# Optimization experiments

Measured on AMD Instinct MI355X. Metric: run time of the kernel, lower is better.

The kernel has to match this reference:

```python
import jax, jax.numpy as jnp
import numpy as np

N_NODES = 50000
N_EDGES = 800000
F_IN = 32      # node_features
F_OUT = 64     # out_channels
K = 3          # filter_size (diffusion steps)
PERIODS = 12


def dconv(X, edge_index, edge_weight, weight, bias):
    """torch_geometric_temporal DConv: dual-direction K-step diffusion conv.
    weight: (2, K, C_in, C_out); direction 0 = out-degree walk, 1 = in-degree walk.
    """
    N = X.shape[0]
    row, col = edge_index[0], edge_index[1]
    # Weighted degrees (edge_weight only enters via degree normalization,
    # matching the original implementation's message = norm * x_j).
    deg_out = jax.ops.segment_sum(edge_weight, row, num_segments=N)
    deg_in = jax.ops.segment_sum(edge_weight, col, num_segments=N)
    norm_out = (1.0 / deg_out)[row]  # [E], rows always have an out-edge here
    norm_in = (1.0 / deg_in)[col]    # [E]

    def prop_fwd(h):  # aggregate along edges src->dst
        return jax.ops.segment_sum(norm_out[:, None] * h[row], col, num_segments=N)

    def prop_rev(h):  # aggregate along reversed edges dst->src
        return jax.ops.segment_sum(norm_in[:, None] * h[col], row, num_segments=N)

    nK = weight.shape[1]
    Tx_0 = X
    H = X @ weight[0, 0] + X @ weight[1, 0]
    if nK > 1:
        Tx_1_o = prop_fwd(X)
        Tx_1_i = prop_rev(X)
        H = H + Tx_1_o @ weight[0, 1] + Tx_1_i @ weight[1, 1]
    for k in range(2, nK):
        Tx_2_o = 2.0 * prop_fwd(Tx_1_o) - Tx_0
        Tx_2_i = 2.0 * prop_rev(Tx_1_i) - Tx_0
        H = H + Tx_2_o @ weight[0, k] + Tx_2_i @ weight[1, k]
        Tx_0, Tx_1_o, Tx_1_i = Tx_1_o, Tx_2_o, Tx_2_i
    return H + bias


def setup_inputs() -> dict:
    key = jax.random.key(0)
    ks = jax.random.split(key, 12)
    C = F_IN + F_OUT  # DConv input channels = cat([X, H])
    s_conv = 1.0 / np.sqrt(C)
    s_lin = 1.0 / np.sqrt(F_OUT)
    return {
        "x": jax.random.normal(ks[0], (N_NODES, F_IN), dtype=jnp.float32),
        "edge_index": jax.random.randint(ks[1], (2, N_EDGES), 0, N_NODES, dtype=jnp.int64) if jax.config.jax_enable_x64 else jax.random.randint(ks[1], (2, N_EDGES), 0, N_NODES, dtype=jnp.int32),
        "edge_weight": jax.random.uniform(ks[2], (N_EDGES,), dtype=jnp.float32, minval=0.05, maxval=1.0),
        "w_z": jax.random.normal(ks[3], (2, K, C, F_OUT), dtype=jnp.float32) * s_conv,
        "b_z": jax.random.normal(ks[4], (F_OUT,), dtype=jnp.float32) * 0.01,
        "w_r": jax.random.normal(ks[5], (2, K, C, F_OUT), dtype=jnp.float32) * s_conv,
        "b_r": jax.random.normal(ks[6], (F_OUT,), dtype=jnp.float32) * 0.01,
        "w_h": jax.random.normal(ks[7], (2, K, C, F_OUT), dtype=jnp.float32) * s_conv,
        "b_h": jax.random.normal(ks[8], (F_OUT,), dtype=jnp.float32) * 0.01,
        "w_lin": jax.random.normal(ks[9], (F_OUT, PERIODS), dtype=jnp.float32) * s_lin,
        "b_lin": jax.random.normal(ks[10], (PERIODS,), dtype=jnp.float32) * s_lin,
    }


def reference(x, edge_index, edge_weight, w_z, b_z, w_r, b_r, w_h, b_h, w_lin, b_lin):
    # DCRNN cell with H0 = zeros (single call, no prior hidden state)
    H0 = jnp.zeros((x.shape[0], F_OUT), dtype=x.dtype)
    xh = jnp.concatenate([x, H0], axis=1)
    Z = jax.nn.sigmoid(dconv(xh, edge_index, edge_weight, w_z, b_z))
    R = jax.nn.sigmoid(dconv(xh, edge_index, edge_weight, w_r, b_r))
    xhr = jnp.concatenate([x, H0 * R], axis=1)
    H_tilde = jnp.tanh(dconv(xhr, edge_index, edge_weight, w_h, b_h))
    H = Z * H0 + (1.0 - Z) * H_tilde
    # ReLU + Linear head
    return jax.nn.relu(H) @ w_lin + b_lin
```

## Files before the change

### kernel.cpp

```cpp
#include <hip/hip_runtime.h>

#define N_NODES 50000
#define N_EDGES 800000
#define F_IN    32
#define F_OUT   64
#define PERIODS 12
#define C_FEAT  160

#define NKEY    (2 * N_NODES)
#define NBIN    782
#define NBLK_A  128
#define EPB     (N_EDGES / NBLK_A)
#define TOT     (2 * N_EDGES)
#define SCANA_N (NBIN * NBLK_A)
#define SCANA_NB 391
#define KPB     16
#define NBLK_DIR (N_NODES / KPB)
#define NF      ((size_t)N_NODES * F_IN)

typedef __attribute__((ext_vector_type(8))) short s16x8;
typedef __attribute__((ext_vector_type(4))) float f32x4;

static __device__ __forceinline__ ushort f2bf(float f) {
    unsigned u = __float_as_uint(f);
    unsigned r = (u + 0x7FFFu + ((u >> 16) & 1u)) >> 16;
    return (ushort)r;
}
static __device__ __forceinline__ float bfLO(unsigned h) {
    return __uint_as_float(h << 16);
}
static __device__ __forceinline__ float bfHI(unsigned h) {
    return __uint_as_float(h & 0xffff0000u);
}

static __device__ __forceinline__ s16x8 pack8(float4 lo, float4 hi) {
    s16x8 r;
    r[0] = (short)f2bf(lo.x); r[1] = (short)f2bf(lo.y);
    r[2] = (short)f2bf(lo.z); r[3] = (short)f2bf(lo.w);
    r[4] = (short)f2bf(hi.x); r[5] = (short)f2bf(hi.y);
    r[6] = (short)f2bf(hi.z); r[7] = (short)f2bf(hi.w);
    return r;
}

__global__ __launch_bounds__(256) void k_histA(const int* __restrict__ ei,
                                               int* __restrict__ hist) {
    __shared__ int h[NBIN];
    int tid = threadIdx.x, blk = blockIdx.x;
    for (int i = tid; i < NBIN; i += 256) h[i] = 0;
    __syncthreads();
    int e0 = blk * EPB;
    for (int i = tid; i < EPB; i += 256) {
        int e = e0 + i;
        int r = ei[e];
        int c = ei[N_EDGES + e];
        atomicAdd(&h[c >> 7], 1);
        atomicAdd(&h[(N_NODES + r) >> 7], 1);
    }
    __syncthreads();
    for (int i = tid; i < NBIN; i += 256) hist[i * NBLK_A + blk] = h[i];
}

__global__ __launch_bounds__(256) void k_scan1(const int* __restrict__ cnt,
                                               int* __restrict__ scanA,
                                               int* __restrict__ bsum) {
    __shared__ int lds[256];
    int g = blockIdx.x * 256 + threadIdx.x;
    int v = (g < SCANA_N) ? cnt[g] : 0;
    int orig = v;
    lds[threadIdx.x] = v;
    __syncthreads();
    for (int d = 1; d < 256; d <<= 1) {
        int t = (threadIdx.x >= d) ? lds[threadIdx.x - d] : 0;
        __syncthreads();
        lds[threadIdx.x] += t;
        __syncthreads();
    }
    if (g < SCANA_N) scanA[g] = lds[threadIdx.x] - orig;
    if (threadIdx.x == 255) bsum[blockIdx.x] = lds[threadIdx.x];
}

__global__ __launch_bounds__(512) void k_scan2(int* __restrict__ bsum) {
    __shared__ int lds[512];
    int t = threadIdx.x;
    int v = (t < SCANA_NB) ? bsum[t] : 0;
    int orig = v;
    lds[t] = v;
    __syncthreads();
    for (int d = 1; d < 512; d <<= 1) {
        int x = (t >= d) ? lds[t - d] : 0;
        __syncthreads();
        lds[t] += x;
        __syncthreads();
    }
    if (t < SCANA_NB) bsum[t] = lds[t] - orig;
}

__global__ __launch_bounds__(256) void k_binA(const int* __restrict__ ei,
                                              const float* __restrict__ ew,
                                              const int* __restrict__ scanA,
                                              const int* __restrict__ bsum,
                                              uint2* __restrict__ binned) {
    __shared__ int cur[NBIN];
    int tid = threadIdx.x, blk = blockIdx.x;
    for (int i = tid; i < NBIN; i += 256) {
        int idx = i * NBLK_A + blk;
        cur[i] = scanA[idx] + bsum[idx >> 8];
    }
    __syncthreads();
    int e0 = blk * EPB;
    for (int i = tid; i < EPB; i += 256) {
        int e = e0 + i;
        int r = ei[e];
        int c = ei[N_EDGES + e];
        unsigned wb = __float_as_uint(ew[e]);
        int k1 = c;
        int k2 = N_NODES + r;
        int p1 = atomicAdd(&cur[k1 >> 7], 1);
        binned[p1] = make_uint2((unsigned)((k1 & 127) | (r << 7)), wb);
        int p2 = atomicAdd(&cur[k2 >> 7], 1);
        binned[p2] = make_uint2((unsigned)((k2 & 127) | (c << 7)), wb);
    }
}

__global__ __launch_bounds__(256) void k_sortbin(const uint2* __restrict__ binned,
                                                 const int* __restrict__ scanA,
                                                 const int* __restrict__ bsum,
                                                 int* __restrict__ csr,
                                                 int* __restrict__ off,
                                                 float* __restrict__ inv) {
    __shared__ int cnt[128];
    __shared__ int sc[128];
    __shared__ int cur[128];
    __shared__ float deg[128];
    int tid = threadIdx.x;
    int b   = blockIdx.x;
    int i0 = b * NBLK_A;
    int base = scanA[i0] + bsum[i0 >> 8];
    int end;
    if (b + 1 < NBIN) {
        int i1 = (b + 1) * NBLK_A;
        end = scanA[i1] + bsum[i1 >> 8];
    } else end = TOT;
    if (tid < 128) { cnt[tid] = 0; deg[tid] = 0.0f; }
    __syncthreads();
    for (int i = base + 2 * tid; i < end; i += 512) {
        uint2 it = binned[i];
        int kl = it.x & 127;
        atomicAdd(&cnt[kl], 1);
        atomicAdd(&deg[kl], __uint_as_float(it.y));
        if (i + 1 < end) {
            uint2 it2 = binned[i + 1];
            int kl2 = it2.x & 127;
            atomicAdd(&cnt[kl2], 1);
            atomicAdd(&deg[kl2], __uint_as_float(it2.y));
        }
    }
    __syncthreads();
    if (tid < 128) sc[tid] = cnt[tid];
    __syncthreads();
    for (int d = 1; d < 128; d <<= 1) {
        int t = (tid >= d && tid < 128) ? sc[tid - d] : 0;
        __syncthreads();
        if (tid < 128) sc[tid] += t;
        __syncthreads();
    }
    if (tid < 128) cur[tid] = sc[tid] - cnt[tid];
    __syncthreads();
    for (int i = base + 2 * tid; i < end; i += 512) {
        uint2 it = binned[i];
        int kl = it.x & 127;
        int pos = atomicAdd(&cur[kl], 1);
        csr[base + pos] = (int)(it.x >> 7);
        if (i + 1 < end) {
            uint2 it2 = binned[i + 1];
            int kl2 = it2.x & 127;
            int pos2 = atomicAdd(&cur[kl2], 1);
            csr[base + pos2] = (int)(it2.x >> 7);
        }
    }
    if (tid < 128) {
        int key = (b << 7) + tid;
        off[key] = base + sc[tid] - cnt[tid];
        inv[key] = 1.0f / deg[tid];
    }
}

__global__ __launch_bounds__(256) void k_xbf(const float* __restrict__ X,
                                             const float* __restrict__ inv,
                                             ushort* __restrict__ Xso,
                                             ushort* __restrict__ Xsi) {
    int t = blockIdx.x * 256 + threadIdx.x;
    if (t * 4 >= (int)NF) return;
    int v = (t * 4) >> 5;
    float so = inv[N_NODES + v];
    float si = inv[v];
    float4 val = *(const float4*)&X[t * 4];
    ushort4 a, b;
    a.x = f2bf(val.x * so); a.y = f2bf(val.y * so);
    a.z = f2bf(val.z * so); a.w = f2bf(val.w * so);
    b.x = f2bf(val.x * si); b.y = f2bf(val.y * si);
    b.z = f2bf(val.z * si); b.w = f2bf(val.w * si);
    *(ushort4*)&Xso[t * 4] = a;
    *(ushort4*)&Xsi[t * 4] = b;
}

template<int STEP>
__global__ __launch_bounds__(256) void k_gather(const int* __restrict__ off,
                                                const int* __restrict__ csr,
                                                const float* __restrict__ inv,
                                                const unsigned* __restrict__ hs_fwd,
                                                const unsigned* __restrict__ hs_rev,
                                                unsigned* __restrict__ raw_fwd,
                                                unsigned* __restrict__ raw_rev,
                                                unsigned* __restrict__ scl_fwd,
                                                unsigned* __restrict__ scl_rev,
                                                float2* __restrict__ f32_fwd,
                                                float2* __restrict__ f32_rev) {
    int g    = blockIdx.x;
    int xcd  = g & 7;
    int slot = g >> 3;
    bool fwd = xcd < 4;
    int blk  = slot * 4 + (xcd & 3);
    if (blk >= NBLK_DIR) return;
    int kg  = threadIdx.x >> 4;
    int f2  = threadIdx.x & 15;
    int key = blk * KPB + kg;
    int idx = fwd ? key : (N_NODES + key);
    const unsigned* hs = fwd ? hs_fwd : hs_rev;
    int beg = off[idx];
    int end = off[idx + 1];
    float aL0 = 0.f, aH0 = 0.f, aL1 = 0.f, aH1 = 0.f;
    int j = beg;
    for (; j + 15 < end; j += 16) {
        int s[16];
#pragma unroll
        for (int u = 0; u < 16; ++u) s[u] = csr[j + u];
        unsigned h[16];
#pragma unroll
        for (int u = 0; u < 16; ++u) h[u] = hs[s[u] * 16 + f2];
#pragma unroll
        for (int u = 0; u < 16; u += 2) {
            aL0 += bfLO(h[u]);     aH0 += bfHI(h[u]);
            aL1 += bfLO(h[u + 1]); aH1 += bfHI(h[u + 1]);
        }
    }
    for (; j + 7 < end; j += 8) {
        int s[8];
#pragma unroll
        for (int u = 0; u < 8; ++u) s[u] = csr[j + u];
        unsigned h[8];
#pragma unroll
        for (int u = 0; u < 8; ++u) h[u] = hs[s[u] * 16 + f2];
#pragma unroll
        for (int u = 0; u < 8; u += 2) {
            aL0 += bfLO(h[u]);     aH0 += bfHI(h[u]);
            aL1 += bfLO(h[u + 1]); aH1 += bfHI(h[u + 1]);
        }
    }
    for (; j + 3 < end; j += 4) {
        int s0 = csr[j], s1 = csr[j + 1], s2 = csr[j + 2], s3 = csr[j + 3];
        unsigned h0 = hs[s0 * 16 + f2], h1 = hs[s1 * 16 + f2];
        unsigned h2 = hs[s2 * 16 + f2], h3 = hs[s3 * 16 + f2];
        aL0 += bfLO(h0); aH0 += bfHI(h0); aL1 += bfLO(h1); aH1 += bfHI(h1);
        aL0 += bfLO(h2); aH0 += bfHI(h2); aL1 += bfLO(h3); aH1 += bfHI(h3);
    }
    for (; j < end; ++j) {
        unsigned h = hs[csr[j] * 16 + f2];
        aL0 += bfLO(h); aH0 += bfHI(h);
    }
    float aL = aL0 + aL1;
    float aH = aH0 + aH1;

    if (STEP == 1) {
        float sc = fwd ? inv[N_NODES + key] : inv[key];
        unsigned raw = ((unsigned)f2bf(aH) << 16) | f2bf(aL);
        unsigned scl = ((unsigned)f2bf(aH * sc) << 16) | f2bf(aL * sc);
        (fwd ? raw_fwd : raw_rev)[key * 16 + f2] = raw;
        (fwd ? scl_fwd : scl_rev)[key * 16 + f2] = scl;
    } else {
        (fwd ? f32_fwd : f32_rev)[key * 16 + f2] = make_float2(aL, aH);
    }
}

__global__ __launch_bounds__(256) void k_prep(const float* __restrict__ wz,
                                              const float* __restrict__ wh,
                                              ushort* __restrict__ Wt) {
    int tid = blockIdx.x * blockDim.x + threadIdx.x;
    if (tid >= 128 * C_FEAT) return;
    int o = tid / C_FEAT;
    int k = tid % C_FEAT;
    int seg = k >> 5;
    int cc  = k & 31;
    const float* src = (o < 64) ? wz : wh;
    int oo = o & 63;
    float val;
    if (seg == 0)      val = src[(0 * 96 + cc) * 64 + oo] + src[(3 * 96 + cc) * 64 + oo];
    else if (seg == 1) val = src[(1 * 96 + cc) * 64 + oo];
    else if (seg == 2) val = src[(4 * 96 + cc) * 64 + oo];
    else if (seg == 3) val = src[(2 * 96 + cc) * 64 + oo];
    else               val = src[(5 * 96 + cc) * 64 + oo];
    Wt[tid] = f2bf(val);
}

__global__ __launch_bounds__(256, 4) void k_final(
        const float* __restrict__ X,
        const ushort* __restrict__ Tx1o,
        const ushort* __restrict__ Tx1i,
        const float* __restrict__ P2o,
        const float* __restrict__ P2i,
        const ushort* __restrict__ Wt,
        const float* __restrict__ bz,
        const float* __restrict__ bh,
        const float* __restrict__ wlin,
        const float* __restrict__ blin,
        float* __restrict__ out) {
    __shared__ float r_lds[32][66];
    int tid   = threadIdx.x;
    int node0 = blockIdx.x * 32;
    int w  = tid >> 6;
    int l  = tid & 63;
    int lr = l & 15;
    int lg = l >> 4;
    int rt = w & 1;
    int cb = (w >> 1) * 32;

    s16x8 bf[4][5];
#pragma unroll
    for (int t = 0; t < 4; ++t) {
        int col = cb + (t & 1) * 16 + lr + ((t >> 1) ? 64 : 0);
        const ushort* wp = Wt + col * C_FEAT + lg * 8;
#pragma unroll
        for (int kb = 0; kb < 5; ++kb)
            bf[t][kb] = *(const s16x8*)(wp + kb * 32);
    }

    int row = node0 + rt * 16 + lr;
    if (row >= N_NODES) row = N_NODES - 1;
    int rbase = row * F_IN + lg * 8;
    float4 x0 = *(const float4*)&X[rbase],   x1 = *(const float4*)&X[rbase + 4];
    float4 p0 = *(const float4*)&P2o[rbase], p1 = *(const float4*)&P2o[rbase + 4];
    float4 q0 = *(const float4*)&P2i[rbase], q1 = *(const float4*)&P2i[rbase + 4];
    s16x8 a[5];
    a[0] = pack8(x0, x1);
    a[1] = *(const s16x8*)&Tx1o[rbase];
    a[2] = *(const s16x8*)&Tx1i[rbase];
    float4 t3l = make_float4(2.f*p0.x-x0.x, 2.f*p0.y-x0.y, 2.f*p0.z-x0.z, 2.f*p0.w-x0.w);
    float4 t3h = make_float4(2.f*p1.x-x1.x, 2.f*p1.y-x1.y, 2.f*p1.z-x1.z, 2.f*p1.w-x1.w);
    float4 t4l = make_float4(2.f*q0.x-x0.x, 2.f*q0.y-x0.y, 2.f*q0.z-x0.z, 2.f*q0.w-x0.w);
    float4 t4h = make_float4(2.f*q1.x-x1.x, 2.f*q1.y-x1.y, 2.f*q1.z-x1.z, 2.f*q1.w-x1.w);
    a[3] = pack8(t3l, t3h);
    a[4] = pack8(t4l, t4h);

    f32x4 acc[4] = {};
#pragma unroll
    for (int kb = 0; kb < 5; ++kb) {
        acc[0] = __builtin_amdgcn_mfma_f32_16x16x32_bf16(a[kb], bf[0][kb], acc[0], 0, 0, 0);
        acc[1] = __builtin_amdgcn_mfma_f32_16x16x32_bf16(a[kb], bf[1][kb], acc[1], 0, 0, 0);
        acc[2] = __builtin_amdgcn_mfma_f32_16x16x32_bf16(a[kb], bf[2][kb], acc[2], 0, 0, 0);
        acc[3] = __builtin_amdgcn_mfma_f32_16x16x32_bf16(a[kb], bf[3][kb], acc[3], 0, 0, 0);
    }

#pragma unroll
    for (int ct = 0; ct < 2; ++ct) {
        int o = cb + ct * 16 + lr;
        float bzv = bz[o];
        float bhv = bh[o];
#pragma unroll
        for (int qq = 0; qq < 4; ++qq) {
            float zp = acc[ct][qq] + bzv;
            float hp = acc[2 + ct][qq] + bhv;
            float z  = 1.0f / (1.0f + __expf(-zp));
            float e2 = __expf(2.0f * hp);
            float th = 1.0f - 2.0f / (e2 + 1.0f);
            r_lds[rt * 16 + lg * 4 + qq][o] = fmaxf((1.0f - z) * th, 0.0f);
        }
    }
    __syncthreads();

    for (int i = tid; i < 32 * PERIODS; i += 256) {
        int n = i / PERIODS;
        int p = i % PERIODS;
        int v = node0 + n;
        if (v < N_NODES) {
            float acc2 = blin[p];
#pragma unroll
            for (int oo = 0; oo < F_OUT; ++oo)
                acc2 = fmaf(r_lds[n][oo], wlin[oo * PERIODS + p], acc2);
            out[v * PERIODS + p] = acc2;
        }
    }
}

extern "C" void kernel_launch(void* const* d_in, const int* in_sizes, int n_in,
                              void* d_out, int out_size, void* d_ws, size_t ws_size,
                              hipStream_t stream) {
    const float* x    = (const float*)d_in[0];
    const int*   ei   = (const int*)d_in[1];
    const float* ew   = (const float*)d_in[2];
    const float* wz   = (const float*)d_in[3];
    const float* bz   = (const float*)d_in[4];
    const float* wh   = (const float*)d_in[7];
    const float* bh   = (const float*)d_in[8];
    const float* wlin = (const float*)d_in[9];
    const float* blin = (const float*)d_in[10];

    int*      histA  = (int*)d_ws;
    int*      scanA  = histA + SCANA_N;
    int*      bsum   = scanA + SCANA_N;
    uint2*    binned = (uint2*)(bsum + 512);
    ushort*   Xso    = (ushort*)binned;
    ushort*   Xsi    = Xso + NF;
    int*      csr    = (int*)(binned + TOT);
    int*      off    = csr + TOT;
    float*    inv    = (float*)(off + 100100);
    ushort*   T1o_b  = (ushort*)(inv + SCANA_N);
    ushort*   T1i_b  = T1o_b + NF;
    ushort*   T1o_s  = T1i_b + NF;
    ushort*   T1i_s  = T1o_s + NF;
    float*    P2o    = (float*)(T1i_s + NF);
    float*    P2i    = P2o + NF;
    ushort*   Wt     = (ushort*)(P2i + NF);

    k_prep<<<(128 * C_FEAT + 255) / 256, 256, 0, stream>>>(wz, wh, Wt);

    k_histA<<<NBLK_A, 256, 0, stream>>>(ei, histA);
    k_scan1<<<SCANA_NB, 256, 0, stream>>>(histA, scanA, bsum);
    k_scan2<<<1, 512, 0, stream>>>(bsum);
    k_binA<<<NBLK_A, 256, 0, stream>>>(ei, ew, scanA, bsum, binned);
    k_sortbin<<<NBIN, 256, 0, stream>>>(binned, scanA, bsum, csr, off, inv);

    k_xbf<<<((int)NF / 4 + 255) / 256, 256, 0, stream>>>(x, inv, Xso, Xsi);

    int ggrid = 8 * ((NBLK_DIR + 3) / 4);
    k_gather<1><<<ggrid, 256, 0, stream>>>(off, csr, inv,
                                           (const unsigned*)Xso, (const unsigned*)Xsi,
                                           (unsigned*)T1o_b, (unsigned*)T1i_b,
                                           (unsigned*)T1o_s, (unsigned*)T1i_s,
                                           nullptr, nullptr);
    k_gather<2><<<ggrid, 256, 0, stream>>>(off, csr, inv,
                                           (const unsigned*)T1o_s, (const unsigned*)T1i_s,
                                           nullptr, nullptr, nullptr, nullptr,
                                           (float2*)P2o, (float2*)P2i);

    k_final<<<(N_NODES + 31) / 32, 256, 0, stream>>>(x, T1o_b, T1i_b, P2o, P2i, Wt,
                                                     bz, bh, wlin, blin, (float*)d_out);
}
```

Before: 133.9 us.

## Fold weight prep into histogram kernel, register-cache sortbin items, nontemporal gathers

Folds the weight-transpose prep kernel into extra blocks of the histogram kernel, removing one launch. In the sort-bin kernel, each thread now holds up to 12 binned items in registers so the scatter pass reuses them instead of re-reading global memory, with a fallback loop for larger bins. The gather kernels switch neighbour-feature loads to nontemporal loads to change cache behaviour. The nontemporal hint may hurt reuse of feature rows that are gathered many times.

```diff
diff --git a/kernel.cpp b/kernel.cpp
--- a/kernel.cpp
+++ b/kernel.cpp
@@ -17,6 +17,7 @@
 #define KPB     16
 #define NBLK_DIR (N_NODES / KPB)
 #define NF      ((size_t)N_NODES * F_IN)
+#define PREP_BLKS ((128 * C_FEAT) / 256)
 
 typedef __attribute__((ext_vector_type(8))) short s16x8;
 typedef __attribute__((ext_vector_type(4))) float f32x4;
@@ -43,9 +44,29 @@
 }
 
 __global__ __launch_bounds__(256) void k_histA(const int* __restrict__ ei,
-                                               int* __restrict__ hist) {
+                                               int* __restrict__ hist,
+                                               const float* __restrict__ wz,
+                                               const float* __restrict__ wh,
+                                               ushort* __restrict__ Wt) {
     __shared__ int h[NBIN];
     int tid = threadIdx.x, blk = blockIdx.x;
+    if (blk >= NBLK_A) {
+        int t = (blk - NBLK_A) * 256 + tid;
+        int o = t / C_FEAT;
+        int k = t % C_FEAT;
+        int seg = k >> 5;
+        int cc  = k & 31;
+        const float* src = (o < 64) ? wz : wh;
+        int oo = o & 63;
+        float val;
+        if (seg == 0)      val = src[(0 * 96 + cc) * 64 + oo] + src[(3 * 96 + cc) * 64 + oo];
+        else if (seg == 1) val = src[(1 * 96 + cc) * 64 + oo];
+        else if (seg == 2) val = src[(4 * 96 + cc) * 64 + oo];
+        else if (seg == 3) val = src[(2 * 96 + cc) * 64 + oo];
+        else               val = src[(5 * 96 + cc) * 64 + oo];
+        Wt[t] = f2bf(val);
+        return;
+    }
     for (int i = tid; i < NBIN; i += 256) h[i] = 0;
     __syncthreads();
     int e0 = blk * EPB;
@@ -143,17 +164,25 @@
     } else end = TOT;
     if (tid < 128) { cnt[tid] = 0; deg[tid] = 0.0f; }
     __syncthreads();
-    for (int i = base + 2 * tid; i < end; i += 512) {
-        uint2 it = binned[i];
-        int kl = it.x & 127;
-        atomicAdd(&cnt[kl], 1);
-        atomicAdd(&deg[kl], __uint_as_float(it.y));
-        if (i + 1 < end) {
-            uint2 it2 = binned[i + 1];
-            int kl2 = it2.x & 127;
-            atomicAdd(&cnt[kl2], 1);
-            atomicAdd(&deg[kl2], __uint_as_float(it2.y));
-        }
+    uint2 it[12];
+#pragma unroll
+    for (int k = 0; k < 12; ++k) {
+        int i = base + tid + k * 256;
+        if (i < end) it[k] = binned[i];
+    }
+#pragma unroll
+    for (int k = 0; k < 12; ++k) {
+        int i = base + tid + k * 256;
+        if (i < end) {
+            int kl = (int)(it[k].x & 127);
+            atomicAdd(&cnt[kl], 1);
+            atomicAdd(&deg[kl], __uint_as_float(it[k].y));
+        }
+    }
+    for (int i = base + 3072 + tid; i < end; i += 256) {
+        uint2 e = binned[i];
+        atomicAdd(&cnt[e.x & 127], 1);
+        atomicAdd(&deg[e.x & 127], __uint_as_float(e.y));
     }
     __syncthreads();
     if (tid < 128) sc[tid] = cnt[tid];
@@ -166,17 +195,19 @@
     }
     if (tid < 128) cur[tid] = sc[tid] - cnt[tid];
     __syncthreads();
-    for (int i = base + 2 * tid; i < end; i += 512) {
-        uint2 it = binned[i];
-        int kl = it.x & 127;
-        int pos = atomicAdd(&cur[kl], 1);
-        csr[base + pos] = (int)(it.x >> 7);
-        if (i + 1 < end) {
-            uint2 it2 = binned[i + 1];
-            int kl2 = it2.x & 127;
-            int pos2 = atomicAdd(&cur[kl2], 1);
-            csr[base + pos2] = (int)(it2.x >> 7);
-        }
+#pragma unroll
+    for (int k = 0; k < 12; ++k) {
+        int i = base + tid + k * 256;
+        if (i < end) {
+            int kl = (int)(it[k].x & 127);
+            int pos = atomicAdd(&cur[kl], 1);
+            csr[base + pos] = (int)(it[k].x >> 7);
+        }
+    }
+    for (int i = base + 3072 + tid; i < end; i += 256) {
+        uint2 e = binned[i];
+        int pos = atomicAdd(&cur[e.x & 127], 1);
+        csr[base + pos] = (int)(e.x >> 7);
     }
     if (tid < 128) {
         int key = (b << 7) + tid;
@@ -237,7 +268,7 @@
         for (int u = 0; u < 16; ++u) s[u] = csr[j + u];
         unsigned h[16];
 #pragma unroll
-        for (int u = 0; u < 16; ++u) h[u] = hs[s[u] * 16 + f2];
+        for (int u = 0; u < 16; ++u) h[u] = __builtin_nontemporal_load(hs + s[u] * 16 + f2);
 #pragma unroll
         for (int u = 0; u < 16; u += 2) {
             aL0 += bfLO(h[u]);     aH0 += bfHI(h[u]);
@@ -250,7 +281,7 @@
         for (int u = 0; u < 8; ++u) s[u] = csr[j + u];
         unsigned h[8];
 #pragma unroll
-        for (int u = 0; u < 8; ++u) h[u] = hs[s[u] * 16 + f2];
+        for (int u = 0; u < 8; ++u) h[u] = __builtin_nontemporal_load(hs + s[u] * 16 + f2);
 #pragma unroll
         for (int u = 0; u < 8; u += 2) {
             aL0 += bfLO(h[u]);     aH0 += bfHI(h[u]);
@@ -259,13 +290,15 @@
     }
     for (; j + 3 < end; j += 4) {
         int s0 = csr[j], s1 = csr[j + 1], s2 = csr[j + 2], s3 = csr[j + 3];
-        unsigned h0 = hs[s0 * 16 + f2], h1 = hs[s1 * 16 + f2];
-        unsigned h2 = hs[s2 * 16 + f2], h3 = hs[s3 * 16 + f2];
+        unsigned h0 = __builtin_nontemporal_load(hs + s0 * 16 + f2);
+        unsigned h1 = __builtin_nontemporal_load(hs + s1 * 16 + f2);
+        unsigned h2 = __builtin_nontemporal_load(hs + s2 * 16 + f2);
+        unsigned h3 = __builtin_nontemporal_load(hs + s3 * 16 + f2);
         aL0 += bfLO(h0); aH0 += bfHI(h0); aL1 += bfLO(h1); aH1 += bfHI(h1);
         aL0 += bfLO(h2); aH0 += bfHI(h2); aL1 += bfLO(h3); aH1 += bfHI(h3);
     }
     for (; j < end; ++j) {
-        unsigned h = hs[csr[j] * 16 + f2];
+        unsigned h = __builtin_nontemporal_load(hs + csr[j] * 16 + f2);
         aL0 += bfLO(h); aH0 += bfHI(h);
     }
     float aL = aL0 + aL1;
@@ -280,26 +313,6 @@
     } else {
         (fwd ? f32_fwd : f32_rev)[key * 16 + f2] = make_float2(aL, aH);
     }
-}
-
-__global__ __launch_bounds__(256) void k_prep(const float* __restrict__ wz,
-                                              const float* __restrict__ wh,
-                                              ushort* __restrict__ Wt) {
-    int tid = blockIdx.x * blockDim.x + threadIdx.x;
-    if (tid >= 128 * C_FEAT) return;
-    int o = tid / C_FEAT;
-    int k = tid % C_FEAT;
-    int seg = k >> 5;
-    int cc  = k & 31;
-    const float* src = (o < 64) ? wz : wh;
-    int oo = o & 63;
-    float val;
-    if (seg == 0)      val = src[(0 * 96 + cc) * 64 + oo] + src[(3 * 96 + cc) * 64 + oo];
-    else if (seg == 1) val = src[(1 * 96 + cc) * 64 + oo];
-    else if (seg == 2) val = src[(4 * 96 + cc) * 64 + oo];
-    else if (seg == 3) val = src[(2 * 96 + cc) * 64 + oo];
-    else               val = src[(5 * 96 + cc) * 64 + oo];
-    Wt[tid] = f2bf(val);
 }
 
 __global__ __launch_bounds__(256, 4) void k_final(
@@ -421,9 +434,7 @@
     float*    P2i    = P2o + NF;
     ushort*   Wt     = (ushort*)(P2i + NF);
 
-    k_prep<<<(128 * C_FEAT + 255) / 256, 256, 0, stream>>>(wz, wh, Wt);
-
-    k_histA<<<NBLK_A, 256, 0, stream>>>(ei, histA);
+    k_histA<<<NBLK_A + PREP_BLKS, 256, 0, stream>>>(ei, histA, wz, wh, Wt);
     k_scan1<<<SCANA_NB, 256, 0, stream>>>(histA, scanA, bsum);
     k_scan2<<<1, 512, 0, stream>>>(bsum);
     k_binA<<<NBLK_A, 256, 0, stream>>>(ei, ew, scanA, bsum, binned);
```

Result: slower. 159.8 us (+19.3%).
